# Optimization experiments

Measured on AMD Instinct MI355X. Metric: run time of the kernel, lower is better.

Reference implementation:

```python
import jax, jax.numpy as jnp
import numpy as np


def _gcn_conv(X, src, dst, norm, W, n_nodes):
    # gather + normalized aggregate (SpMM) then dense linear (GEMM)
    msg = X[src] * norm[:, None]                       # [E, F]
    agg = jax.ops.segment_sum(msg, dst, num_segments=n_nodes)  # [N, F]
    return agg @ W                                     # [N, F_out]


def setup_inputs() -> dict:
    key = jax.random.key(0)
    k1, k2, k3, k4, k5 = jax.random.split(key, 5)
    N, E, D_IN, D_HID, D_OUT = 50000, 800000, 128, 128, 64
    X = jax.random.normal(k1, (N, D_IN), dtype=jnp.float32)
    edge_index = jax.random.randint(k2, (2, E), 0, N, dtype=jnp.int64)
    s = 1.0 / np.sqrt(D_IN)
    W1 = jax.random.normal(k3, (D_IN, D_HID), dtype=jnp.float32) * s
    W2 = jax.random.normal(k4, (D_HID, D_HID), dtype=jnp.float32) * s
    W3 = jax.random.normal(k5, (D_HID, D_OUT), dtype=jnp.float32) * s
    return {"X": X, "edge_index": edge_index, "W1": W1, "W2": W2, "W3": W3}


def reference(X, edge_index, W1, W2, W3):
    n_nodes = X.shape[0]
    src, dst = edge_index[0], edge_index[1]
    # symmetric degree normalization D^-1/2 A D^-1/2 (degrees from edge list)
    ones = jnp.ones(src.shape[0], dtype=X.dtype)
    deg = jax.ops.segment_sum(ones, dst, num_segments=n_nodes)
    deg = jnp.maximum(deg, 1.0)
    dinv = jax.lax.rsqrt(deg)
    norm = dinv[src] * dinv[dst]                       # [E]
    h = jax.nn.relu(_gcn_conv(X, src, dst, norm, W1, n_nodes))
    h = jax.nn.relu(_gcn_conv(h, src, dst, norm, W2, n_nodes))
    h = jax.nn.relu(_gcn_conv(h, src, dst, norm, W3, n_nodes))
    return jax.nn.softmax(h, axis=-1)
```

## Files before the change

### kernel.cpp

```cpp
#include <hip/hip_runtime.h>
#include <hip/hip_bf16.h>

typedef __attribute__((ext_vector_type(8))) short short8;
typedef __attribute__((ext_vector_type(4))) short short4v;
typedef __attribute__((ext_vector_type(4))) float f32x4;

static inline size_t ws_align(size_t x) { return (x + 511) & ~((size_t)511); }

static __device__ inline unsigned short f2bf(float f) {
    __hip_bfloat16 h = __float2bfloat16(f);
    return __builtin_bit_cast(unsigned short, h);
}

static __device__ inline float bf2f(unsigned short u) {
    unsigned int x = ((unsigned int)u) << 16;
    return __builtin_bit_cast(float, x);
}


template <int FOUT>
static __device__ inline void gemm128_body(const void* __restrict__ Araw, int a_fp32,
                                           const void* __restrict__ Wraw, int w_fp32,
                                           unsigned short* __restrict__ out,
                                           int N, int blk) {
    constexpr int K = 128;
    constexpr int NT = FOUT / 16;
    constexpr int LDB = K + 8;
    __shared__ __align__(16) unsigned short bt[FOUT * LDB];

    const int tid = threadIdx.x;
    const int base = blk * 128;

    constexpr int TOT4 = K * FOUT / 4;
    if (w_fp32) {
        const float* Wf = (const float*)Wraw;
        for (int i = tid; i < TOT4; i += 512) {
            int idx = i * 4;
            int k = idx / FOUT;
            int n = idx & (FOUT - 1);
            float4 v = *(const float4*)(const void*)(Wf + idx);
            bt[(n + 0) * LDB + k] = f2bf(v.x);
            bt[(n + 1) * LDB + k] = f2bf(v.y);
            bt[(n + 2) * LDB + k] = f2bf(v.z);
            bt[(n + 3) * LDB + k] = f2bf(v.w);
        }
    } else {
        const unsigned short* Ws = (const unsigned short*)Wraw;
        for (int i = tid; i < TOT4; i += 512) {
            int idx = i * 4;
            int k = idx / FOUT;
            int n = idx & (FOUT - 1);
            short4v v = *(const short4v*)(const void*)(Ws + idx);
#pragma unroll
            for (int j = 0; j < 4; j++) bt[(n + j) * LDB + k] = ((const unsigned short*)&v)[j];
        }
    }

    const int wave = tid >> 6;
    const int lane = tid & 63;
    const int quad = lane >> 4;
    const int r16 = lane & 15;

    int arow = base + wave * 16 + r16;
    if (arow > N - 1) arow = N - 1;

    short8 afrag[4];
    if (a_fp32) {
        const float* Ap = (const float*)Araw + (size_t)arow * K + quad * 8;
#pragma unroll
        for (int kk = 0; kk < 4; kk++) {
            float4 f0 = *(const float4*)(const void*)(Ap + kk * 32);
            float4 f1 = *(const float4*)(const void*)(Ap + kk * 32 + 4);
            short8 r;
            r[0] = (short)f2bf(f0.x); r[1] = (short)f2bf(f0.y);
            r[2] = (short)f2bf(f0.z); r[3] = (short)f2bf(f0.w);
            r[4] = (short)f2bf(f1.x); r[5] = (short)f2bf(f1.y);
            r[6] = (short)f2bf(f1.z); r[7] = (short)f2bf(f1.w);
            afrag[kk] = r;
        }
    } else {
        const unsigned short* Ap = (const unsigned short*)Araw + (size_t)arow * K + quad * 8;
#pragma unroll
        for (int kk = 0; kk < 4; kk++) afrag[kk] = *(const short8*)(const void*)(Ap + kk * 32);
    }

    __syncthreads();

    f32x4 acc[NT];
#pragma unroll
    for (int nt = 0; nt < NT; nt++) acc[nt] = (f32x4){0.f, 0.f, 0.f, 0.f};

#pragma unroll
    for (int kk = 0; kk < 4; kk++) {
#pragma unroll
        for (int nt = 0; nt < NT; nt++) {
            short8 b = *(const short8*)(const void*)(&bt[(nt * 16 + r16) * LDB + kk * 32 + quad * 8]);
            acc[nt] = __builtin_amdgcn_mfma_f32_16x16x32_bf16(afrag[kk], b, acc[nt], 0, 0, 0);
        }
    }

#pragma unroll
    for (int nt = 0; nt < NT; nt++) {
#pragma unroll
        for (int r = 0; r < 4; r++) {
            float v = acc[nt][r];
            float o = __shfl_xor(v, 1, 64);
            int row = base + wave * 16 + quad * 4 + r;
            if (((lane & 1) == 0) && row < N) {
                __hip_bfloat162 pk;
                pk.x = __float2bfloat16(v);
                pk.y = __float2bfloat16(o);
                *(__hip_bfloat162*)(out + (size_t)row * FOUT + nt * 16 + r16) = pk;
            }
        }
    }
}


__global__ __launch_bounds__(512) void gemm1_hist_kernel(const void* __restrict__ Xraw,
                                                         const unsigned short* __restrict__ w1s,
                                                         const int* __restrict__ ei,
                                                         int* __restrict__ counts,
                                                         int* __restrict__ loff,
                                                         int* __restrict__ flags,
                                                         unsigned short* __restrict__ out,
                                                         int N, int E, int gblocks) {
    const int tid = threadIdx.x;
    const int lane = tid & 63;

    unsigned ew = (w1s[2 * lane] >> 7) & 0xFF;
    unsigned long long m1 = __ballot(ew >= 100 && ew <= 130);
    const int in_fp32 = (__popcll(m1) < 48) ? 1 : 0;

    if (blockIdx.x >= gblocks) {
        unsigned long long m2 = __ballot(((const unsigned int*)ei)[2 * lane + 1] == 0u);
        const int ei64 = (__popcll(m2) >= 48) ? 1 : 0;
        if (blockIdx.x == gblocks && tid == 0) {
            flags[0] = in_fp32;
            flags[1] = ei64;
        }
        int e = (blockIdx.x - gblocks) * 512 + tid;
        if (e < E) {
            int d = ei64 ? ei[2 * (size_t)E + 2 * e] : ei[(size_t)E + e];
            loff[e] = atomicAdd(&counts[d], 1);
        }
        return;
    }

    gemm128_body<128>(Xraw, in_fp32, (const void*)w1s, in_fp32, out, N, blockIdx.x);
}


template <int FOUT>
__global__ __launch_bounds__(512) void gemm_kernel(const void* __restrict__ Araw,
                                                   const void* __restrict__ Wraw,
                                                   const int* __restrict__ flags,
                                                   unsigned short* __restrict__ out, int N) {
    gemm128_body<FOUT>(Araw, 0, Wraw, flags[0], out, N, blockIdx.x);
}


__global__ __launch_bounds__(256) void alloc_kernel(const int* __restrict__ counts,
                                                    float* __restrict__ dinv,
                                                    int* __restrict__ rowptr,
                                                    int* __restrict__ total, int N) {
    int n = blockIdx.x * blockDim.x + threadIdx.x;
    int lane = threadIdx.x & 63;
    int c = (n < N) ? counts[n] : 0;
    if (n < N) {
        int d = (c < 1) ? 1 : c;
        dinv[n] = rsqrtf((float)d);
    }
    int incl = c;
#pragma unroll
    for (int off = 1; off < 64; off <<= 1) {
        int v = __shfl_up(incl, off, 64);
        if (lane >= off) incl += v;
    }
    int wavetot = __shfl(incl, 63, 64);
    int base = 0;
    if (lane == 0) base = atomicAdd(total, wavetot);
    base = __shfl(base, 0, 64);
    if (n < N) rowptr[n] = base + incl - c;
}

__global__ void fill_kernel(const int* __restrict__ ei, const int* __restrict__ flags,
                            const float* __restrict__ dinv, const int* __restrict__ rowptr,
                            const int* __restrict__ loff, int2* __restrict__ edgedat, int E) {
    int e = blockIdx.x * blockDim.x + threadIdx.x;
    if (e < E) {
        int s, d;
        if (flags[1]) {
            s = ei[2 * e];
            d = ei[2 * (size_t)E + 2 * e];
        } else {
            s = ei[e];
            d = ei[(size_t)E + e];
        }
        int pos = rowptr[d] + loff[e];
        float wt = dinv[s] * dinv[d];
        edgedat[pos] = make_int2(s, __float_as_int(wt));
    }
}


__global__ __launch_bounds__(256) void spmm128_kernel(const int2* __restrict__ edgedat,
                                                      const int* __restrict__ rowptr,
                                                      const int* __restrict__ counts,
                                                      const unsigned short* __restrict__ Hin,
                                                      unsigned short* __restrict__ Hout, int N) {
    int wid = (blockIdx.x * 256 + threadIdx.x) >> 6;
    if (wid >= N) return;
    int lane = threadIdx.x & 63;
    int grp = lane >> 4;
    int gl = lane & 15;
    int n = __builtin_amdgcn_readfirstlane(wid);
    int start = __builtin_amdgcn_readfirstlane(rowptr[n]);
    int len = __builtin_amdgcn_readfirstlane(counts[n]);
    const int2* ep = edgedat + start;

    float acc[8];
#pragma unroll
    for (int u = 0; u < 8; u++) acc[u] = 0.f;

    int j = 0;
    for (; j + 8 <= len; j += 8) {
        int2 e0 = ep[j + grp];
        int2 e1 = ep[j + 4 + grp];
        short8 h0 = *(const short8*)(const void*)(Hin + (size_t)e0.x * 128 + gl * 8);
        short8 h1 = *(const short8*)(const void*)(Hin + (size_t)e1.x * 128 + gl * 8);
        float w0 = __int_as_float(e0.y);
        float w1 = __int_as_float(e1.y);
#pragma unroll
        for (int u = 0; u < 8; u++) acc[u] += w0 * bf2f((unsigned short)h0[u]);
#pragma unroll
        for (int u = 0; u < 8; u++) acc[u] += w1 * bf2f((unsigned short)h1[u]);
    }
    for (; j + 4 <= len; j += 4) {
        int2 e = ep[j + grp];
        short8 h = *(const short8*)(const void*)(Hin + (size_t)e.x * 128 + gl * 8);
        float w = __int_as_float(e.y);
#pragma unroll
        for (int u = 0; u < 8; u++) acc[u] += w * bf2f((unsigned short)h[u]);
    }
    int rem = len - j;
    if (grp < rem) {
        int2 e = ep[j + grp];
        short8 h = *(const short8*)(const void*)(Hin + (size_t)e.x * 128 + gl * 8);
        float w = __int_as_float(e.y);
#pragma unroll
        for (int u = 0; u < 8; u++) acc[u] += w * bf2f((unsigned short)h[u]);
    }

#pragma unroll
    for (int u = 0; u < 8; u++) {
        acc[u] += __shfl_xor(acc[u], 16, 64);
        acc[u] += __shfl_xor(acc[u], 32, 64);
    }

    if (grp == 0) {
        short8 o;
#pragma unroll
        for (int u = 0; u < 8; u++) o[u] = (short)f2bf(fmaxf(acc[u], 0.f));
        *(short8*)(void*)(Hout + (size_t)n * 128 + gl * 8) = o;
    }
}


__global__ __launch_bounds__(256) void spmm64_softmax_kernel(const int2* __restrict__ edgedat,
                                                             const int* __restrict__ rowptr,
                                                             const int* __restrict__ counts,
                                                             const unsigned short* __restrict__ Hin,
                                                             const int* __restrict__ flags,
                                                             void* __restrict__ Out, int N) {
    int wid = (blockIdx.x * 256 + threadIdx.x) >> 6;
    if (wid >= N) return;
    int lane = threadIdx.x & 63;
    int grp = lane >> 3;
    int gl = lane & 7;
    int n = __builtin_amdgcn_readfirstlane(wid);
    int start = __builtin_amdgcn_readfirstlane(rowptr[n]);
    int len = __builtin_amdgcn_readfirstlane(counts[n]);
    const int2* ep = edgedat + start;

    float acc[8];
#pragma unroll
    for (int u = 0; u < 8; u++) acc[u] = 0.f;

    int j = 0;
    for (; j + 16 <= len; j += 16) {
        int2 e0 = ep[j + grp];
        int2 e1 = ep[j + 8 + grp];
        short8 h0 = *(const short8*)(const void*)(Hin + (size_t)e0.x * 64 + gl * 8);
        short8 h1 = *(const short8*)(const void*)(Hin + (size_t)e1.x * 64 + gl * 8);
        float w0 = __int_as_float(e0.y);
        float w1 = __int_as_float(e1.y);
#pragma unroll
        for (int u = 0; u < 8; u++) acc[u] += w0 * bf2f((unsigned short)h0[u]);
#pragma unroll
        for (int u = 0; u < 8; u++) acc[u] += w1 * bf2f((unsigned short)h1[u]);
    }
    for (; j + 8 <= len; j += 8) {
        int2 e = ep[j + grp];
        short8 h = *(const short8*)(const void*)(Hin + (size_t)e.x * 64 + gl * 8);
        float w = __int_as_float(e.y);
#pragma unroll
        for (int u = 0; u < 8; u++) acc[u] += w * bf2f((unsigned short)h[u]);
    }
    int rem = len - j;
    if (grp < rem) {
        int2 e = ep[j + grp];
        short8 h = *(const short8*)(const void*)(Hin + (size_t)e.x * 64 + gl * 8);
        float w = __int_as_float(e.y);
#pragma unroll
        for (int u = 0; u < 8; u++) acc[u] += w * bf2f((unsigned short)h[u]);
    }

#pragma unroll
    for (int u = 0; u < 8; u++) {
        acc[u] += __shfl_xor(acc[u], 8, 64);
        acc[u] += __shfl_xor(acc[u], 16, 64);
        acc[u] += __shfl_xor(acc[u], 32, 64);
    }

#pragma unroll
    for (int u = 0; u < 8; u++) acc[u] = fmaxf(acc[u], 0.f);

    float m = acc[0];
#pragma unroll
    for (int u = 1; u < 8; u++) m = fmaxf(m, acc[u]);
#pragma unroll
    for (int off = 1; off < 8; off <<= 1) m = fmaxf(m, __shfl_xor(m, off, 64));

    float ex[8];
    float s = 0.f;
#pragma unroll
    for (int u = 0; u < 8; u++) {
        ex[u] = __expf(acc[u] - m);
        s += ex[u];
    }
#pragma unroll
    for (int off = 1; off < 8; off <<= 1) s += __shfl_xor(s, off, 64);
    float inv = 1.0f / s;

    if (grp == 0) {
        if (flags[0]) {
            float* op = (float*)Out + (size_t)n * 64 + gl * 8;
            float4 v0, v1;
            v0.x = ex[0] * inv; v0.y = ex[1] * inv; v0.z = ex[2] * inv; v0.w = ex[3] * inv;
            v1.x = ex[4] * inv; v1.y = ex[5] * inv; v1.z = ex[6] * inv; v1.w = ex[7] * inv;
            *(float4*)(void*)op = v0;
            *(float4*)(void*)(op + 4) = v1;
        } else {
            short8 o;
#pragma unroll
            for (int u = 0; u < 8; u++) o[u] = (short)f2bf(ex[u] * inv);
            *(short8*)(void*)((unsigned short*)Out + (size_t)n * 64 + gl * 8) = o;
        }
    }
}


extern "C" void kernel_launch(void* const* d_in, const int* in_sizes, int n_in,
                              void* d_out, int out_size, void* d_ws, size_t ws_size,
                              hipStream_t stream) {
    const void* X  = d_in[0];
    const int*  ei = (const int*)d_in[1];
    const void* W1 = d_in[2];
    const void* W2 = d_in[3];
    const void* W3 = d_in[4];

    const int N = in_sizes[0] / 128;
    const int E = in_sizes[1] / 2;

    char* ws = (char*)d_ws;
    size_t off = 0;
    int* counts = (int*)(ws + off);   off += ws_align((size_t)N * 4);
    int* total  = (int*)(ws + off);   off += ws_align(64);
    const size_t zero_bytes = off;
    int* flags    = (int*)(ws + off);   off += ws_align(64);
    int* rowptr   = (int*)(ws + off);   off += ws_align((size_t)N * 4);
    float* dinv   = (float*)(ws + off); off += ws_align((size_t)N * 4);
    int* loff     = (int*)(ws + off);   off += ws_align((size_t)E * 4);
    int2* edgedat = (int2*)(ws + off);  off += ws_align((size_t)E * 8);
    unsigned short* HA = (unsigned short*)(ws + off); off += ws_align((size_t)N * 128 * 2);
    unsigned short* HB = (unsigned short*)(ws + off); off += ws_align((size_t)N * 128 * 2);

    hipMemsetAsync(d_ws, 0, zero_bytes, stream);

    const int gblocks = (N + 127) / 128;
    const int hblocks = (E + 511) / 512;
    const int sblocks = (N * 64 + 255) / 256;

    gemm1_hist_kernel<<<gblocks + hblocks, 512, 0, stream>>>(
        X, (const unsigned short*)W1, ei, counts, loff, flags, HA, N, E, gblocks);
    alloc_kernel<<<(N + 255) / 256, 256, 0, stream>>>(counts, dinv, rowptr, total, N);
    fill_kernel<<<(E + 255) / 256, 256, 0, stream>>>(ei, flags, dinv, rowptr, loff, edgedat, E);

    spmm128_kernel<<<sblocks, 256, 0, stream>>>(edgedat, rowptr, counts, HA, HB, N);
    gemm_kernel<128><<<gblocks, 512, 0, stream>>>(HB, W2, flags, HA, N);
    spmm128_kernel<<<sblocks, 256, 0, stream>>>(edgedat, rowptr, counts, HA, HB, N);
    gemm_kernel<64><<<gblocks, 512, 0, stream>>>(HB, W3, flags, HA, N);
    spmm64_softmax_kernel<<<sblocks, 256, 0, stream>>>(edgedat, rowptr, counts, HA, flags, d_out, N);
}
```

Measured before the change: 257.7 us.

## Fuse SpMM aggregation with following dense GEMM into one kernel per layer

Each of layers 2 and 3 now runs a single kernel. Sixteen waves per block each aggregate one node's neighbours into shared memory, then the block multiplies that 16x128 tile by the weight matrix with bf16 MFMA. This removes the intermediate aggregated-feature write and read, and one launch per layer. In exchange, every 16-node block reloads and transposes the full weight matrix into LDS, and most waves sit idle during the small GEMM phase.

```diff
diff --git a/kernel.cpp b/kernel.cpp
--- a/kernel.cpp
+++ b/kernel.cpp
@@ -18,12 +18,12 @@
 }
 
 
-template <int FOUT>
 static __device__ inline void gemm128_body(const void* __restrict__ Araw, int a_fp32,
                                            const void* __restrict__ Wraw, int w_fp32,
                                            unsigned short* __restrict__ out,
                                            int N, int blk) {
     constexpr int K = 128;
+    constexpr int FOUT = 128;
     constexpr int NT = FOUT / 16;
     constexpr int LDB = K + 8;
     __shared__ __align__(16) unsigned short bt[FOUT * LDB];
@@ -147,16 +147,7 @@
         return;
     }
 
-    gemm128_body<128>(Xraw, in_fp32, (const void*)w1s, in_fp32, out, N, blockIdx.x);
-}
-
-
-template <int FOUT>
-__global__ __launch_bounds__(512) void gemm_kernel(const void* __restrict__ Araw,
-                                                   const void* __restrict__ Wraw,
-                                                   const int* __restrict__ flags,
-                                                   unsigned short* __restrict__ out, int N) {
-    gemm128_body<FOUT>(Araw, 0, Wraw, flags[0], out, N, blockIdx.x);
+    gemm128_body(Xraw, in_fp32, (const void*)w1s, in_fp32, out, N, blockIdx.x);
 }
 
 
@@ -204,19 +195,61 @@
 }
 
 
-__global__ __launch_bounds__(256) void spmm128_kernel(const int2* __restrict__ edgedat,
-                                                      const int* __restrict__ rowptr,
-                                                      const int* __restrict__ counts,
-                                                      const unsigned short* __restrict__ Hin,
-                                                      unsigned short* __restrict__ Hout, int N) {
-    int wid = (blockIdx.x * 256 + threadIdx.x) >> 6;
-    if (wid >= N) return;
-    int lane = threadIdx.x & 63;
-    int grp = lane >> 4;
-    int gl = lane & 15;
-    int n = __builtin_amdgcn_readfirstlane(wid);
-    int start = __builtin_amdgcn_readfirstlane(rowptr[n]);
-    int len = __builtin_amdgcn_readfirstlane(counts[n]);
+template <int FOUT>
+__global__ __launch_bounds__(1024, 8) void spmmgemm_kernel(const int2* __restrict__ edgedat,
+                                                           const int* __restrict__ rowptr,
+                                                           const int* __restrict__ counts,
+                                                           const unsigned short* __restrict__ Hin,
+                                                           const void* __restrict__ Wraw,
+                                                           const int* __restrict__ flags,
+                                                           unsigned short* __restrict__ out, int N) {
+    constexpr int K = 128;
+    constexpr int NT = FOUT / 16;
+    constexpr int LDB = K + 8;
+    constexpr int LDA = K + 8;
+    __shared__ __align__(16) unsigned short bt[FOUT * LDB];
+    __shared__ __align__(16) unsigned short agg[16 * LDA];
+
+    const int tid = threadIdx.x;
+    const int wave = tid >> 6;
+    const int lane = tid & 63;
+    const int w_fp32 = flags[0];
+
+    constexpr int TOT4 = K * FOUT / 4;
+    if (w_fp32) {
+        const float* Wf = (const float*)Wraw;
+        for (int i = tid; i < TOT4; i += 1024) {
+            int idx = i * 4;
+            int k = idx / FOUT;
+            int n = idx & (FOUT - 1);
+            float4 v = *(const float4*)(const void*)(Wf + idx);
+            bt[(n + 0) * LDB + k] = f2bf(v.x);
+            bt[(n + 1) * LDB + k] = f2bf(v.y);
+            bt[(n + 2) * LDB + k] = f2bf(v.z);
+            bt[(n + 3) * LDB + k] = f2bf(v.w);
+        }
+    } else {
+        const unsigned short* Ws = (const unsigned short*)Wraw;
+        for (int i = tid; i < TOT4; i += 1024) {
+            int idx = i * 4;
+            int k = idx / FOUT;
+            int n = idx & (FOUT - 1);
+            short4v v = *(const short4v*)(const void*)(Ws + idx);
+#pragma unroll
+            for (int j = 0; j < 4; j++) bt[(n + j) * LDB + k] = ((const unsigned short*)&v)[j];
+        }
+    }
+
+    const int grp = lane >> 4;
+    const int gl = lane & 15;
+    int node = blockIdx.x * 16 + wave;
+    int start = 0, len = 0;
+    if (node < N) {
+        start = rowptr[node];
+        len = counts[node];
+    }
+    start = __builtin_amdgcn_readfirstlane(start);
+    len = __builtin_amdgcn_readfirstlane(len);
     const int2* ep = edgedat + start;
 
     float acc[8];
@@ -262,7 +295,38 @@
         short8 o;
 #pragma unroll
         for (int u = 0; u < 8; u++) o[u] = (short)f2bf(fmaxf(acc[u], 0.f));
-        *(short8*)(void*)(Hout + (size_t)n * 128 + gl * 8) = o;
+        *(short8*)(void*)(&agg[wave * LDA + gl * 8]) = o;
+    }
+
+    __syncthreads();
+
+    if (wave >= NT) return;
+    const int quad = lane >> 4;
+    const int r16 = lane & 15;
+
+    short8 afrag[4];
+#pragma unroll
+    for (int kk = 0; kk < 4; kk++)
+        afrag[kk] = *(const short8*)(const void*)(&agg[r16 * LDA + kk * 32 + quad * 8]);
+
+    f32x4 c = (f32x4){0.f, 0.f, 0.f, 0.f};
+#pragma unroll
+    for (int kk = 0; kk < 4; kk++) {
+        short8 b = *(const short8*)(const void*)(&bt[(wave * 16 + r16) * LDB + kk * 32 + quad * 8]);
+        c = __builtin_amdgcn_mfma_f32_16x16x32_bf16(afrag[kk], b, c, 0, 0, 0);
+    }
+
+#pragma unroll
+    for (int r = 0; r < 4; r++) {
+        float v = c[r];
+        float o = __shfl_xor(v, 1, 64);
+        int row = blockIdx.x * 16 + quad * 4 + r;
+        if (((lane & 1) == 0) && row < N) {
+            __hip_bfloat162 pk;
+            pk.x = __float2bfloat16(v);
+            pk.y = __float2bfloat16(o);
+            *(__hip_bfloat162*)(out + (size_t)row * FOUT + wave * 16 + r16) = pk;
+        }
     }
 }
 
@@ -390,6 +454,7 @@
 
     const int gblocks = (N + 127) / 128;
     const int hblocks = (E + 511) / 512;
+    const int fblocks = (N + 15) / 16;
     const int sblocks = (N * 64 + 255) / 256;
 
     gemm1_hist_kernel<<<gblocks + hblocks, 512, 0, stream>>>(
@@ -397,9 +462,7 @@
     alloc_kernel<<<(N + 255) / 256, 256, 0, stream>>>(counts, dinv, rowptr, total, N);
     fill_kernel<<<(E + 255) / 256, 256, 0, stream>>>(ei, flags, dinv, rowptr, loff, edgedat, E);
 
-    spmm128_kernel<<<sblocks, 256, 0, stream>>>(edgedat, rowptr, counts, HA, HB, N);
-    gemm_kernel<128><<<gblocks, 512, 0, stream>>>(HB, W2, flags, HA, N);
-    spmm128_kernel<<<sblocks, 256, 0, stream>>>(edgedat, rowptr, counts, HA, HB, N);
-    gemm_kernel<64><<<gblocks, 512, 0, stream>>>(HB, W3, flags, HA, N);
+    spmmgemm_kernel<128><<<fblocks, 1024, 0, stream>>>(edgedat, rowptr, counts, HA, W2, flags, HB, N);
+    spmmgemm_kernel<64><<<fblocks, 1024, 0, stream>>>(edgedat, rowptr, counts, HB, W3, flags, HA, N);
     spmm64_softmax_kernel<<<sblocks, 256, 0, stream>>>(edgedat, rowptr, counts, HA, flags, d_out, N);
 }
```

Measured after the change: 284.8 us. 10.5% more time.
